# Kernel optimization log

Hardware: AMD Instinct MI355X
Metric: run time of the kernel (lower is better)

Reference implementation:

```python
import jax, jax.numpy as jnp
import numpy as np

B, T, E, D, G = 64, 64, 2048, 4096, 8
H3 = 3 * D  # gru projects deter -> 3*deter (reset, cand, update)
EPS = 1e-4  # Norm default eps


def _rms(x, scale):
    # Norm impl='rms': x * rsqrt(mean(x^2, -1) + eps) * scale
    return x * (jax.lax.rsqrt((x * x).mean(-1, keepdims=True) + EPS) * scale)


def setup_inputs() -> dict:
    key = jax.random.key(0)
    ks = jax.random.split(key, 4)
    x = jax.random.normal(ks[0], (B, T, E), jnp.float32)
    deter0 = jax.random.normal(ks[1], (B, D), jnp.float32)
    # dense in-projection: concat(deter, x) -> D, rms norm + silu
    W_in = jax.random.normal(ks[2], (D + E, D), jnp.float32) * (1.0 / np.sqrt(D + E))
    b_in = jnp.zeros((D,), jnp.float32)
    scale_in = jnp.ones((D,), jnp.float32)
    # BlockLinear D -> 3D with G groups; weight (G, D/G, 3D/G), per-block rms scales
    W_blk = jax.random.normal(ks[3], (G, D // G, H3 // G), jnp.float32) * (1.0 / np.sqrt(D // G))
    b_blk = jnp.zeros((H3,), jnp.float32)
    scale_blk = jnp.ones((G, H3 // G), jnp.float32)
    return dict(x=x, deter0=deter0, W_in=W_in, b_in=b_in, scale_in=scale_in,
                W_blk=W_blk, b_blk=b_blk, scale_blk=scale_blk)


def reference(x, deter0, W_in, b_in, scale_in, W_blk, b_blk, scale_blk):
    def step(deter, x_t):
        h = jnp.concatenate([deter, x_t], -1)                # [B, D+E]
        y = jax.nn.silu(_rms(h @ W_in + b_in, scale_in))     # [B, D]
        # block-diagonal GEMM: '...ki,kio->...ko' as in BlockLinear._layer
        z = jnp.einsum('bgi,gio->bgo', y.reshape(B, G, D // G), W_blk)
        z = z.reshape(B, H3) + b_blk
        # block_norm=True: per-block rms over each of the G contiguous chunks
        z = _rms(z.reshape(B, G, H3 // G), scale_blk).reshape(B, H3)
        reset, cand, update = jnp.split(z, 3, -1)
        reset = jax.nn.sigmoid(reset)
        cand = jnp.tanh(reset * cand)
        update = jax.nn.sigmoid(update - 1.0)
        deter = update * cand + (1.0 - update) * deter
        return deter, deter

    _, deters = jax.lax.scan(step, deter0, jnp.swapaxes(x, 0, 1))  # scan over T
    return jnp.swapaxes(deters, 0, 1)  # [B, T, D]
```

## Files before the change

kernel.cpp:

```cpp
#include <hip/hip_runtime.h>

typedef unsigned short u16;
typedef unsigned int u32;
typedef __bf16 bfx8 __attribute__((ext_vector_type(8)));
typedef float f32x4 __attribute__((ext_vector_type(4)));

constexpr int BB = 64;
constexpr int TT = 64;
constexpr int EE = 2048;
constexpr int DD = 4096;
constexpr int GG = 8;
constexpr int H3 = 3 * DD;
constexpr int CH = H3 / GG;
constexpr float EPSf = 1e-4f;

static __device__ __forceinline__ u16 f2bf(float f) {
  u32 u = __builtin_bit_cast(u32, f);
  u32 r = (u + 0x7fffu + ((u >> 16) & 1u)) >> 16;
  return (u16)r;
}
static __device__ __forceinline__ float bf2f(u16 h) {
  return __builtin_bit_cast(float, (u32)h << 16);
}


__global__ void __launch_bounds__(256) k_f2b(const float* __restrict__ in,
                                             u16* __restrict__ out, int n4) {
  int i = blockIdx.x * 256 + threadIdx.x;
  int stride = gridDim.x * 256;
  for (; i < n4; i += stride) {
    float4 v = ((const float4*)in)[i];
    uint2 o;
    o.x = (u32)f2bf(v.x) | ((u32)f2bf(v.y) << 16);
    o.y = (u32)f2bf(v.z) | ((u32)f2bf(v.w) << 16);
    ((uint2*)out)[i] = o;
  }
}

__global__ void __launch_bounds__(256) k_initdet(const float* __restrict__ d0,
                                                 float* __restrict__ dF,
                                                 u16* __restrict__ dB, int n4) {
  int i = blockIdx.x * 256 + threadIdx.x;
  if (i < n4) {
    float4 v = ((const float4*)d0)[i];
    ((float4*)dF)[i] = v;
    uint2 o;
    o.x = (u32)f2bf(v.x) | ((u32)f2bf(v.y) << 16);
    o.y = (u32)f2bf(v.z) | ((u32)f2bf(v.w) << 16);
    ((uint2*)dB)[i] = o;
  }
}

__global__ void __launch_bounds__(256) k_transpose_f2b(const float* __restrict__ in,
                                                       u16* __restrict__ out,
                                                       int R, int C) {
  __shared__ float tile[32][33];
  size_t base = (size_t)blockIdx.z * R * C;
  in += base; out += base;
  int tx = threadIdx.x & 31, ty = threadIdx.x >> 5;
  int r0 = blockIdx.y * 32, c0 = blockIdx.x * 32;
#pragma unroll
  for (int i = 0; i < 4; i++) {
    int rr = ty * 4 + i;
    tile[rr][tx] = in[(size_t)(r0 + rr) * C + (c0 + tx)];
  }
  __syncthreads();
#pragma unroll
  for (int i = 0; i < 4; i++) {
    int cc = ty * 4 + i;
    out[(size_t)(c0 + cc) * R + (r0 + tx)] = f2bf(tile[tx][cc]);
  }
}

constexpr int P1_LS = 72;
constexpr int P1_BUF = 128 * P1_LS;

__global__ void __launch_bounds__(256) k_p1(const u16* __restrict__ A,
                                            const u16* __restrict__ B,
                                            const float* __restrict__ bias,
                                            u16* __restrict__ C) {
  __shared__ u16 As[2 * P1_BUF];
  __shared__ u16 Bs[2 * P1_BUF];
  const int tid = threadIdx.x;
  const int m0 = blockIdx.y * 128, n0 = blockIdx.x * 128;
  const int w = tid >> 6, lane = tid & 63;
  const int wr = w >> 1, wc = w & 1;
  const int lr = lane & 15, lk = (lane >> 4) * 8, rq = (lane >> 4) * 4;
  const int srow = tid >> 3, scol = (tid & 7) * 8;
  const u16* Ag = A + (size_t)(m0 + srow) * EE + scol;
  const u16* Bg = B + (size_t)(n0 + srow) * (DD + EE) + scol;

  f32x4 acc[4][4] = {};
  uint4 ra[4], rb[4];
#pragma unroll
  for (int i = 0; i < 4; i++) {
    ra[i] = *(const uint4*)(Ag + (size_t)32 * i * EE);
    rb[i] = *(const uint4*)(Bg + (size_t)32 * i * (DD + EE));
  }

  for (int kt = 0; kt < 32; ++kt) {
    const int p = kt & 1;
    u16* ab = As + p * P1_BUF;
    u16* bb = Bs + p * P1_BUF;
#pragma unroll
    for (int i = 0; i < 4; i++) {
      *(uint4*)&ab[(srow + 32 * i) * P1_LS + scol] = ra[i];
      *(uint4*)&bb[(srow + 32 * i) * P1_LS + scol] = rb[i];
    }
    __syncthreads();
    if (kt < 31) {
      const int ko = (kt + 1) * 64;
#pragma unroll
      for (int i = 0; i < 4; i++) {
        ra[i] = *(const uint4*)(Ag + (size_t)32 * i * EE + ko);
        rb[i] = *(const uint4*)(Bg + (size_t)32 * i * (DD + EE) + ko);
      }
    }
#pragma unroll
    for (int kk = 0; kk < 64; kk += 32) {
      bfx8 av[4], bv[4];
#pragma unroll
      for (int mi = 0; mi < 4; mi++)
        av[mi] = *(const bfx8*)&ab[(wr * 64 + mi * 16 + lr) * P1_LS + kk + lk];
#pragma unroll
      for (int ni = 0; ni < 4; ni++)
        bv[ni] = *(const bfx8*)&bb[(wc * 64 + ni * 16 + lr) * P1_LS + kk + lk];
#pragma unroll
      for (int mi = 0; mi < 4; mi++)
#pragma unroll
        for (int ni = 0; ni < 4; ni++)
          acc[mi][ni] = __builtin_amdgcn_mfma_f32_16x16x32_bf16(av[mi], bv[ni], acc[mi][ni], 0, 0, 0);
    }
  }

#pragma unroll
  for (int mi = 0; mi < 4; mi++) {
#pragma unroll
    for (int ni = 0; ni < 4; ni++) {
      const int n = n0 + wc * 64 + ni * 16 + lr;
      const float bias_v = bias[n];
#pragma unroll
      for (int r = 0; r < 4; r++) {
        const int m = m0 + wr * 64 + mi * 16 + rq + r;
        C[(size_t)m * DD + n] = f2bf(acc[mi][ni][r] + bias_v);
      }
    }
  }
}

constexpr int LSA = 136;
constexpr int ABUF = 64 * LSA;

__global__ void __launch_bounds__(512) kA(const u16* __restrict__ dB,
                                          const u16* __restrict__ WT,
                                          float* __restrict__ part) {
  __shared__ u16 As[2 * ABUF];
  __shared__ u16 Bs[2 * ABUF];
  const int tid = threadIdx.x;
  const int n0 = blockIdx.x * 64;
  const int k0 = blockIdx.y * 1024;
  const int w = tid >> 6, lane = tid & 63;
  const int wr = w >> 1, wc = w & 1;
  const int lr = lane & 15, lk = (lane >> 4) * 8, rq = (lane >> 4) * 4;
  const int r0s = tid >> 4, s0 = (tid & 15) * 8;
  const int r1s = r0s + 32;
  const u16* Ag0 = dB + (size_t)r0s * DD + k0 + s0;
  const u16* Ag1 = dB + (size_t)r1s * DD + k0 + s0;
  const u16* Bg0 = WT + (size_t)(n0 + r0s) * (DD + EE) + k0 + s0;
  const u16* Bg1 = WT + (size_t)(n0 + r1s) * (DD + EE) + k0 + s0;
  const int d0 = r0s * LSA + s0, d1 = r1s * LSA + s0;

  f32x4 acc[2] = {};
  uint4 ra0 = *(const uint4*)(Ag0);
  uint4 ra1 = *(const uint4*)(Ag1);
  uint4 rb0 = *(const uint4*)(Bg0);
  uint4 rb1 = *(const uint4*)(Bg1);

  for (int kt = 0; kt < 8; ++kt) {
    const int p = kt & 1;
    u16* ab = As + p * ABUF;
    u16* bb = Bs + p * ABUF;
    *(uint4*)&ab[d0] = ra0;
    *(uint4*)&ab[d1] = ra1;
    *(uint4*)&bb[d0] = rb0;
    *(uint4*)&bb[d1] = rb1;
    __syncthreads();
    if (kt < 7) {
      const int ko = (kt + 1) * 128;
      ra0 = *(const uint4*)(Ag0 + ko);
      ra1 = *(const uint4*)(Ag1 + ko);
      rb0 = *(const uint4*)(Bg0 + ko);
      rb1 = *(const uint4*)(Bg1 + ko);
    }
#pragma unroll
    for (int kk = 0; kk < 128; kk += 32) {
      bfx8 av = *(const bfx8*)&ab[(wr * 16 + lr) * LSA + kk + lk];
#pragma unroll
      for (int ni = 0; ni < 2; ni++) {
        bfx8 bv = *(const bfx8*)&bb[(wc * 32 + ni * 16 + lr) * LSA + kk + lk];
        acc[ni] = __builtin_amdgcn_mfma_f32_16x16x32_bf16(av, bv, acc[ni], 0, 0, 0);
      }
    }
  }

  float* Pp = part + (size_t)blockIdx.y * BB * DD;
#pragma unroll
  for (int ni = 0; ni < 2; ni++)
#pragma unroll
    for (int r = 0; r < 4; r++)
      Pp[(size_t)(wr * 16 + rq + r) * DD + n0 + wc * 32 + ni * 16 + lr] = acc[ni][r];
}

__global__ void __launch_bounds__(256) kB(const float* __restrict__ part,
                                          const u16* __restrict__ Xproj,
                                          const float* __restrict__ scale_in,
                                          u16* __restrict__ ybf, int t) {
  const int b = blockIdx.x, tid = threadIdx.x;
  const int w = tid >> 6, lane = tid & 63;
  __shared__ float sred[4];
  const u16* xp = Xproj + ((size_t)b * TT + t) * DD + tid * 16;
  const float* pb = part + (size_t)b * DD + tid * 16;
  float v[16];
  uint4 x0 = *(const uint4*)(xp);
  uint4 x1 = *(const uint4*)(xp + 8);
#pragma unroll
  for (int j = 0; j < 8; j++) v[j] = bf2f(((const u16*)&x0)[j]);
#pragma unroll
  for (int j = 0; j < 8; j++) v[8 + j] = bf2f(((const u16*)&x1)[j]);
#pragma unroll
  for (int kc = 0; kc < 4; kc++) {
    const float* p = pb + (size_t)kc * BB * DD;
#pragma unroll
    for (int j4 = 0; j4 < 4; j4++) {
      float4 q = *(const float4*)(p + j4 * 4);
      v[j4 * 4 + 0] += q.x; v[j4 * 4 + 1] += q.y;
      v[j4 * 4 + 2] += q.z; v[j4 * 4 + 3] += q.w;
    }
  }
  float ss = 0.f;
#pragma unroll
  for (int j = 0; j < 16; j++) ss += v[j] * v[j];
#pragma unroll
  for (int o = 32; o > 0; o >>= 1) ss += __shfl_down(ss, o);
  if (lane == 0) sred[w] = ss;
  __syncthreads();
  const float r = rsqrtf((sred[0] + sred[1] + sred[2] + sred[3]) / (float)DD + EPSf);
  const float* sc = scale_in + tid * 16;
  uint2 o0, o1;
  u32* po = (u32*)&o0;
#pragma unroll
  for (int j = 0; j < 4; j++) {
    float a = v[2 * j] * r * sc[2 * j];
    float bq = v[2 * j + 1] * r * sc[2 * j + 1];
    a = a / (1.f + __expf(-a)); bq = bq / (1.f + __expf(-bq));
    po[j & 1] = (u32)f2bf(a) | ((u32)f2bf(bq) << 16);
    if (j == 1) *(uint2*)(ybf + (size_t)b * DD + tid * 16) = o0;
  }
  *(uint2*)(ybf + (size_t)b * DD + tid * 16 + 4) = o0;
  u32 pk[8];
#pragma unroll
  for (int j = 0; j < 8; j++) {
    float a = v[2 * j] * r * sc[2 * j];
    float bq = v[2 * j + 1] * r * sc[2 * j + 1];
    a = a / (1.f + __expf(-a)); bq = bq / (1.f + __expf(-bq));
    pk[j] = (u32)f2bf(a) | ((u32)f2bf(bq) << 16);
  }
  uint4 w0 = make_uint4(pk[0], pk[1], pk[2], pk[3]);
  uint4 w1 = make_uint4(pk[4], pk[5], pk[6], pk[7]);
  *(uint4*)(ybf + (size_t)b * DD + tid * 16) = w0;
  *(uint4*)(ybf + (size_t)b * DD + tid * 16 + 8) = w1;
}

constexpr int LSC2 = 72;
constexpr int CBUF = 64 * LSC2;

__global__ void __launch_bounds__(256) kC(const u16* __restrict__ ybf,
                                          const u16* __restrict__ WbT,
                                          const float* __restrict__ b_blk,
                                          float* __restrict__ zbuf,
                                          float* __restrict__ zsq) {
  __shared__ u16 As[2 * CBUF];
  __shared__ u16 Bs[2 * CBUF];
  const int tid = threadIdx.x;
  const int wg = blockIdx.x;
  const int n0g = wg * 64;
  const int g = n0g / CH, nl = n0g % CH;
  const int w = tid >> 6, lane = tid & 63;
  const int lr = lane & 15, lk = (lane >> 4) * 8, rq = (lane >> 4) * 4;
  const int srow = tid >> 2, sc = (tid & 3) * 8;
  const u16* Arow = ybf + (size_t)srow * DD + g * (DD / GG) + sc;
  const u16* Brow = WbT + ((size_t)g * CH + nl + srow) * (DD / GG) + sc;
  const int dA = srow * LSC2 + sc;

  f32x4 acc[4] = {};
  uint4 ra0 = *(const uint4*)(Arow);
  uint4 ra1 = *(const uint4*)(Arow + 32);
  uint4 rb0 = *(const uint4*)(Brow);
  uint4 rb1 = *(const uint4*)(Brow + 32);

  for (int kt = 0; kt < 8; ++kt) {
    const int p = kt & 1;
    u16* ab = As + p * CBUF;
    u16* bb = Bs + p * CBUF;
    *(uint4*)&ab[dA] = ra0;
    *(uint4*)&ab[dA + 32] = ra1;
    *(uint4*)&bb[dA] = rb0;
    *(uint4*)&bb[dA + 32] = rb1;
    __syncthreads();
    if (kt < 7) {
      const int ko = (kt + 1) * 64;
      ra0 = *(const uint4*)(Arow + ko);
      ra1 = *(const uint4*)(Arow + ko + 32);
      rb0 = *(const uint4*)(Brow + ko);
      rb1 = *(const uint4*)(Brow + ko + 32);
    }
#pragma unroll
    for (int kk = 0; kk < 64; kk += 32) {
      bfx8 av = *(const bfx8*)&ab[(w * 16 + lr) * LSC2 + kk + lk];
#pragma unroll
      for (int ni = 0; ni < 4; ni++) {
        bfx8 bv = *(const bfx8*)&bb[(ni * 16 + lr) * LSC2 + kk + lk];
        acc[ni] = __builtin_amdgcn_mfma_f32_16x16x32_bf16(av, bv, acc[ni], 0, 0, 0);
      }
    }
  }

  float sq[4] = {0.f, 0.f, 0.f, 0.f};
#pragma unroll
  for (int ni = 0; ni < 4; ni++) {
    const int n = n0g + ni * 16 + lr;
    const float bias_v = b_blk[n];
#pragma unroll
    for (int r = 0; r < 4; r++) {
      const float zv = acc[ni][r] + bias_v;
      zbuf[(size_t)(w * 16 + rq + r) * H3 + n] = zv;
      sq[r] += zv * zv;
    }
  }
#pragma unroll
  for (int o = 1; o < 16; o <<= 1) {
#pragma unroll
    for (int r = 0; r < 4; r++) sq[r] += __shfl_xor(sq[r], o);
  }
  if (lr == 0) {
#pragma unroll
    for (int r = 0; r < 4; r++) zsq[(size_t)wg * 64 + w * 16 + rq + r] = sq[r];
  }
}

__global__ void __launch_bounds__(256) kD(const float* __restrict__ zbuf,
                                          const float* __restrict__ zsq,
                                          const float* __restrict__ sblk,
                                          float* __restrict__ dF,
                                          u16* __restrict__ dB,
                                          float* __restrict__ out, int t) {
  const int wg = blockIdx.x, tid = threadIdx.x;
  const int b = wg >> 2, s = wg & 3;
  __shared__ float sred[8];
  if (tid < 8) {
    float ssq = 0.f;
    const int j0 = tid * 24;
#pragma unroll
    for (int j = 0; j < 24; j++) ssq += zsq[(size_t)(j0 + j) * 64 + b];
    sred[tid] = rsqrtf(ssq / (float)CH + EPSf);
  }
  __syncthreads();
  const int d0 = s * 1024 + tid * 4;
  const float* zr = zbuf + (size_t)b * H3;
  float4 z0 = *(const float4*)(zr + d0);
  float4 z1 = *(const float4*)(zr + DD + d0);
  float4 z2 = *(const float4*)(zr + 2 * DD + d0);
  float4 dold = *(const float4*)(dF + (size_t)b * DD + d0);
  const float rsA = sred[d0 / CH];
  const float rsB = sred[(DD + d0) / CH];
  const float rsC = sred[(2 * DD + d0) / CH];
  float dn[4];
  const float* z0p = (const float*)&z0;
  const float* z1p = (const float*)&z1;
  const float* z2p = (const float*)&z2;
  const float* dop = (const float*)&dold;
#pragma unroll
  for (int e = 0; e < 4; e++) {
    const int dd = d0 + e;
    const float a0 = z0p[e] * rsA * sblk[dd];
    const float a1 = z1p[e] * rsB * sblk[DD + dd];
    const float a2 = z2p[e] * rsC * sblk[2 * DD + dd];
    const float reset = 1.f / (1.f + __expf(-a0));
    const float cand = tanhf(reset * a1);
    const float upd = 1.f / (1.f + __expf(-(a2 - 1.f)));
    dn[e] = upd * cand + (1.f - upd) * dop[e];
  }
  *(float4*)(dF + (size_t)b * DD + d0) = make_float4(dn[0], dn[1], dn[2], dn[3]);
  uint2 o;
  o.x = (u32)f2bf(dn[0]) | ((u32)f2bf(dn[1]) << 16);
  o.y = (u32)f2bf(dn[2]) | ((u32)f2bf(dn[3]) << 16);
  *(uint2*)(dB + (size_t)b * DD + d0) = o;
  *(float4*)(out + ((size_t)b * TT + t) * DD + d0) = make_float4(dn[0], dn[1], dn[2], dn[3]);
}


extern "C" void kernel_launch(void* const* d_in, const int* in_sizes, int n_in,
                              void* d_out, int out_size, void* d_ws, size_t ws_size,
                              hipStream_t stream) {
  (void)in_sizes; (void)n_in; (void)out_size; (void)ws_size;
  const float* x         = (const float*)d_in[0];
  const float* deter0    = (const float*)d_in[1];
  const float* W_in      = (const float*)d_in[2];
  const float* b_in      = (const float*)d_in[3];
  const float* scale_in  = (const float*)d_in[4];
  const float* W_blk     = (const float*)d_in[5];
  const float* b_blk     = (const float*)d_in[6];
  const float* scale_blk = (const float*)d_in[7];
  float* out = (float*)d_out;

  char* ws = (char*)d_ws;
  size_t off = 0;
  auto alloc = [&](size_t bytes) -> void* {
    void* p = ws + off;
    off += (bytes + 255) & ~(size_t)255;
    return p;
  };
  u16*   WT    = (u16*)alloc((size_t)DD * (DD + EE) * 2);
  u16*   WbT   = (u16*)alloc((size_t)GG * CH * (DD / GG) * 2);
  u16*   Xproj = (u16*)alloc((size_t)BB * TT * DD * 2);
  float* dF    = (float*)alloc((size_t)BB * DD * 4);
  u16*   dB    = (u16*)alloc((size_t)BB * DD * 2);
  char* scratch = (char*)alloc((size_t)BB * TT * EE * 2);
  u16*   xbf  = (u16*)scratch;
  float* part = (float*)scratch;
  size_t o2 = (size_t)4 * BB * DD * 4;
  u16*   ybf  = (u16*)(scratch + o2);
  o2 += (size_t)BB * DD * 2;
  float* zbuf = (float*)(scratch + o2);
  o2 += (size_t)BB * H3 * 4;
  float* zsq  = (float*)(scratch + o2);

  k_f2b<<<dim3(2048), dim3(256), 0, stream>>>(x, xbf, BB * TT * EE / 4);
  k_transpose_f2b<<<dim3(DD / 32, (DD + EE) / 32, 1), dim3(256), 0, stream>>>(W_in, WT, DD + EE, DD);
  k_transpose_f2b<<<dim3(CH / 32, (DD / GG) / 32, GG), dim3(256), 0, stream>>>(W_blk, WbT, DD / GG, CH);
  k_initdet<<<dim3(BB * DD / 4 / 256), dim3(256), 0, stream>>>(deter0, dF, dB, BB * DD / 4);

  k_p1<<<dim3(DD / 128, BB * TT / 128), dim3(256), 0, stream>>>(
      xbf, WT + DD, b_in, Xproj);

  for (int t = 0; t < TT; t++) {
    kA<<<dim3(64, 4), dim3(512), 0, stream>>>(dB, WT, part);
    kB<<<dim3(BB), dim3(256), 0, stream>>>(part, Xproj, scale_in, ybf, t);
    kC<<<dim3(192), dim3(256), 0, stream>>>(ybf, WbT, b_blk, zbuf, zsq);
    kD<<<dim3(256), dim3(256), 0, stream>>>(zbuf, zsq, scale_blk, dF, dB, out, t);
  }
}
```

Baseline: 1.999 ms.

## Fuse per-step recurrent kernels into one persistent kernel with grid barriers

Replaces the 256 per-timestep kernel launches (four kernels times 64 steps) with a single persistent kernel of 256 workgroups. The four phases run in a loop and are separated by atomic-counter grid barriers that are zeroed once up front. Phase A is retiled to 256-thread workgroups covering 64x64 outputs with a 16-step K loop so it matches the common block shape. This removes launch gaps and kernel-boundary drains, but it relies on all 256 workgroups being co-resident and adds spin-wait barrier cost; phase A also loses its 512-thread parallelism.

```diff
diff --git a/kernel.cpp b/kernel.cpp
--- a/kernel.cpp
+++ b/kernel.cpp
@@ -49,6 +49,11 @@
     o.y = (u32)f2bf(v.z) | ((u32)f2bf(v.w) << 16);
     ((uint2*)dB)[i] = o;
   }
+}
+
+__global__ void __launch_bounds__(256) k_zero(int* __restrict__ p, int n) {
+  int i = blockIdx.x * 256 + threadIdx.x;
+  if (i < n) p[i] = 0;
 }
 
 __global__ void __launch_bounds__(256) k_transpose_f2b(const float* __restrict__ in,
@@ -148,149 +153,48 @@
   }
 }
 
-constexpr int LSA = 136;
-constexpr int ABUF = 64 * LSA;
-
-__global__ void __launch_bounds__(512) kA(const u16* __restrict__ dB,
-                                          const u16* __restrict__ WT,
-                                          float* __restrict__ part) {
-  __shared__ u16 As[2 * ABUF];
-  __shared__ u16 Bs[2 * ABUF];
-  const int tid = threadIdx.x;
-  const int n0 = blockIdx.x * 64;
-  const int k0 = blockIdx.y * 1024;
-  const int w = tid >> 6, lane = tid & 63;
-  const int wr = w >> 1, wc = w & 1;
-  const int lr = lane & 15, lk = (lane >> 4) * 8, rq = (lane >> 4) * 4;
-  const int r0s = tid >> 4, s0 = (tid & 15) * 8;
-  const int r1s = r0s + 32;
-  const u16* Ag0 = dB + (size_t)r0s * DD + k0 + s0;
-  const u16* Ag1 = dB + (size_t)r1s * DD + k0 + s0;
-  const u16* Bg0 = WT + (size_t)(n0 + r0s) * (DD + EE) + k0 + s0;
-  const u16* Bg1 = WT + (size_t)(n0 + r1s) * (DD + EE) + k0 + s0;
-  const int d0 = r0s * LSA + s0, d1 = r1s * LSA + s0;
-
-  f32x4 acc[2] = {};
-  uint4 ra0 = *(const uint4*)(Ag0);
-  uint4 ra1 = *(const uint4*)(Ag1);
-  uint4 rb0 = *(const uint4*)(Bg0);
-  uint4 rb1 = *(const uint4*)(Bg1);
-
-  for (int kt = 0; kt < 8; ++kt) {
-    const int p = kt & 1;
-    u16* ab = As + p * ABUF;
-    u16* bb = Bs + p * ABUF;
-    *(uint4*)&ab[d0] = ra0;
-    *(uint4*)&ab[d1] = ra1;
-    *(uint4*)&bb[d0] = rb0;
-    *(uint4*)&bb[d1] = rb1;
-    __syncthreads();
-    if (kt < 7) {
-      const int ko = (kt + 1) * 128;
-      ra0 = *(const uint4*)(Ag0 + ko);
-      ra1 = *(const uint4*)(Ag1 + ko);
-      rb0 = *(const uint4*)(Bg0 + ko);
-      rb1 = *(const uint4*)(Bg1 + ko);
-    }
-#pragma unroll
-    for (int kk = 0; kk < 128; kk += 32) {
-      bfx8 av = *(const bfx8*)&ab[(wr * 16 + lr) * LSA + kk + lk];
-#pragma unroll
-      for (int ni = 0; ni < 2; ni++) {
-        bfx8 bv = *(const bfx8*)&bb[(wc * 32 + ni * 16 + lr) * LSA + kk + lk];
-        acc[ni] = __builtin_amdgcn_mfma_f32_16x16x32_bf16(av, bv, acc[ni], 0, 0, 0);
-      }
-    }
-  }
-
-  float* Pp = part + (size_t)blockIdx.y * BB * DD;
-#pragma unroll
-  for (int ni = 0; ni < 2; ni++)
-#pragma unroll
-    for (int r = 0; r < 4; r++)
-      Pp[(size_t)(wr * 16 + rq + r) * DD + n0 + wc * 32 + ni * 16 + lr] = acc[ni][r];
-}
-
-__global__ void __launch_bounds__(256) kB(const float* __restrict__ part,
-                                          const u16* __restrict__ Xproj,
-                                          const float* __restrict__ scale_in,
-                                          u16* __restrict__ ybf, int t) {
-  const int b = blockIdx.x, tid = threadIdx.x;
-  const int w = tid >> 6, lane = tid & 63;
-  __shared__ float sred[4];
-  const u16* xp = Xproj + ((size_t)b * TT + t) * DD + tid * 16;
-  const float* pb = part + (size_t)b * DD + tid * 16;
-  float v[16];
-  uint4 x0 = *(const uint4*)(xp);
-  uint4 x1 = *(const uint4*)(xp + 8);
-#pragma unroll
-  for (int j = 0; j < 8; j++) v[j] = bf2f(((const u16*)&x0)[j]);
-#pragma unroll
-  for (int j = 0; j < 8; j++) v[8 + j] = bf2f(((const u16*)&x1)[j]);
-#pragma unroll
-  for (int kc = 0; kc < 4; kc++) {
-    const float* p = pb + (size_t)kc * BB * DD;
-#pragma unroll
-    for (int j4 = 0; j4 < 4; j4++) {
-      float4 q = *(const float4*)(p + j4 * 4);
-      v[j4 * 4 + 0] += q.x; v[j4 * 4 + 1] += q.y;
-      v[j4 * 4 + 2] += q.z; v[j4 * 4 + 3] += q.w;
-    }
-  }
-  float ss = 0.f;
-#pragma unroll
-  for (int j = 0; j < 16; j++) ss += v[j] * v[j];
-#pragma unroll
-  for (int o = 32; o > 0; o >>= 1) ss += __shfl_down(ss, o);
-  if (lane == 0) sred[w] = ss;
+
+struct SPc {
+  const u16* WT;
+  const u16* WbT;
+  const u16* Xproj;
+  const float* scale_in;
+  const float* b_blk;
+  const float* sblk;
+  float* part;
+  u16* ybf;
+  float* zbuf;
+  float* zsq;
+  float* dF;
+  u16* dB;
+  float* out;
+  int* bars;
+};
+
+static __device__ __forceinline__ void gbar(int* cnt, int target) {
   __syncthreads();
-  const float r = rsqrtf((sred[0] + sred[1] + sred[2] + sred[3]) / (float)DD + EPSf);
-  const float* sc = scale_in + tid * 16;
-  uint2 o0, o1;
-  u32* po = (u32*)&o0;
-#pragma unroll
-  for (int j = 0; j < 4; j++) {
-    float a = v[2 * j] * r * sc[2 * j];
-    float bq = v[2 * j + 1] * r * sc[2 * j + 1];
-    a = a / (1.f + __expf(-a)); bq = bq / (1.f + __expf(-bq));
-    po[j & 1] = (u32)f2bf(a) | ((u32)f2bf(bq) << 16);
-    if (j == 1) *(uint2*)(ybf + (size_t)b * DD + tid * 16) = o0;
-  }
-  *(uint2*)(ybf + (size_t)b * DD + tid * 16 + 4) = o0;
-  u32 pk[8];
-#pragma unroll
-  for (int j = 0; j < 8; j++) {
-    float a = v[2 * j] * r * sc[2 * j];
-    float bq = v[2 * j + 1] * r * sc[2 * j + 1];
-    a = a / (1.f + __expf(-a)); bq = bq / (1.f + __expf(-bq));
-    pk[j] = (u32)f2bf(a) | ((u32)f2bf(bq) << 16);
-  }
-  uint4 w0 = make_uint4(pk[0], pk[1], pk[2], pk[3]);
-  uint4 w1 = make_uint4(pk[4], pk[5], pk[6], pk[7]);
-  *(uint4*)(ybf + (size_t)b * DD + tid * 16) = w0;
-  *(uint4*)(ybf + (size_t)b * DD + tid * 16 + 8) = w1;
-}
-
-constexpr int LSC2 = 72;
-constexpr int CBUF = 64 * LSC2;
-
-__global__ void __launch_bounds__(256) kC(const u16* __restrict__ ybf,
-                                          const u16* __restrict__ WbT,
-                                          const float* __restrict__ b_blk,
-                                          float* __restrict__ zbuf,
-                                          float* __restrict__ zsq) {
-  __shared__ u16 As[2 * CBUF];
-  __shared__ u16 Bs[2 * CBUF];
-  const int tid = threadIdx.x;
-  const int wg = blockIdx.x;
-  const int n0g = wg * 64;
-  const int g = n0g / CH, nl = n0g % CH;
+  if (threadIdx.x == 0) {
+    __hip_atomic_fetch_add(cnt, 1, __ATOMIC_RELEASE, __HIP_MEMORY_SCOPE_AGENT);
+    while (__hip_atomic_load(cnt, __ATOMIC_RELAXED, __HIP_MEMORY_SCOPE_AGENT) < target)
+      __builtin_amdgcn_s_sleep(4);
+  }
+  __syncthreads();
+  __builtin_amdgcn_fence(__ATOMIC_ACQUIRE, "agent");
+}
+
+constexpr int LSS = 72;
+constexpr int SBUF = 64 * LSS;
+
+static __device__ __forceinline__ void phaseA(const SPc& P, int wg, int tid,
+                                              u16* As, u16* Bs) {
+  const int n0 = (wg & 63) * 64;
+  const int k0 = (wg >> 6) * 1024;
   const int w = tid >> 6, lane = tid & 63;
   const int lr = lane & 15, lk = (lane >> 4) * 8, rq = (lane >> 4) * 4;
   const int srow = tid >> 2, sc = (tid & 3) * 8;
-  const u16* Arow = ybf + (size_t)srow * DD + g * (DD / GG) + sc;
-  const u16* Brow = WbT + ((size_t)g * CH + nl + srow) * (DD / GG) + sc;
-  const int dA = srow * LSC2 + sc;
+  const u16* Arow = P.dB + (size_t)srow * DD + k0 + sc;
+  const u16* Brow = P.WT + (size_t)(n0 + srow) * (DD + EE) + k0 + sc;
+  const int dA = srow * LSS + sc;
 
   f32x4 acc[4] = {};
   uint4 ra0 = *(const uint4*)(Arow);
@@ -298,10 +202,107 @@
   uint4 rb0 = *(const uint4*)(Brow);
   uint4 rb1 = *(const uint4*)(Brow + 32);
 
+  for (int kt = 0; kt < 16; ++kt) {
+    const int p = kt & 1;
+    u16* ab = As + p * SBUF;
+    u16* bb = Bs + p * SBUF;
+    *(uint4*)&ab[dA] = ra0;
+    *(uint4*)&ab[dA + 32] = ra1;
+    *(uint4*)&bb[dA] = rb0;
+    *(uint4*)&bb[dA + 32] = rb1;
+    __syncthreads();
+    if (kt < 15) {
+      const int ko = (kt + 1) * 64;
+      ra0 = *(const uint4*)(Arow + ko);
+      ra1 = *(const uint4*)(Arow + ko + 32);
+      rb0 = *(const uint4*)(Brow + ko);
+      rb1 = *(const uint4*)(Brow + ko + 32);
+    }
+#pragma unroll
+    for (int kk = 0; kk < 64; kk += 32) {
+      bfx8 av = *(const bfx8*)&ab[(w * 16 + lr) * LSS + kk + lk];
+#pragma unroll
+      for (int ni = 0; ni < 4; ni++) {
+        bfx8 bv = *(const bfx8*)&bb[(ni * 16 + lr) * LSS + kk + lk];
+        acc[ni] = __builtin_amdgcn_mfma_f32_16x16x32_bf16(av, bv, acc[ni], 0, 0, 0);
+      }
+    }
+  }
+
+  float* Pp = P.part + (size_t)(wg >> 6) * BB * DD;
+#pragma unroll
+  for (int ni = 0; ni < 4; ni++)
+#pragma unroll
+    for (int r = 0; r < 4; r++)
+      Pp[(size_t)(w * 16 + rq + r) * DD + n0 + ni * 16 + lr] = acc[ni][r];
+}
+
+static __device__ __forceinline__ void phaseB(const SPc& P, int b, int tid, int t,
+                                              float* sred) {
+  const int w = tid >> 6, lane = tid & 63;
+  const u16* xp = P.Xproj + ((size_t)b * TT + t) * DD + tid * 16;
+  const float* pb = P.part + (size_t)b * DD + tid * 16;
+  float v[16];
+  uint4 x0 = *(const uint4*)(xp);
+  uint4 x1 = *(const uint4*)(xp + 8);
+#pragma unroll
+  for (int j = 0; j < 8; j++) {
+    v[j] = bf2f(((const u16*)&x0)[j]);
+    v[8 + j] = bf2f(((const u16*)&x1)[j]);
+  }
+#pragma unroll
+  for (int kc = 0; kc < 4; kc++) {
+    const float* p = pb + (size_t)kc * BB * DD;
+#pragma unroll
+    for (int j4 = 0; j4 < 4; j4++) {
+      float4 q = *(const float4*)(p + j4 * 4);
+      v[j4 * 4 + 0] += q.x; v[j4 * 4 + 1] += q.y;
+      v[j4 * 4 + 2] += q.z; v[j4 * 4 + 3] += q.w;
+    }
+  }
+  float ss = 0.f;
+#pragma unroll
+  for (int j = 0; j < 16; j++) ss += v[j] * v[j];
+#pragma unroll
+  for (int o = 32; o > 0; o >>= 1) ss += __shfl_down(ss, o);
+  if (lane == 0) sred[w] = ss;
+  __syncthreads();
+  const float r = rsqrtf((sred[0] + sred[1] + sred[2] + sred[3]) / (float)DD + EPSf);
+  const float* sc = P.scale_in + tid * 16;
+  u32 pk[8];
+#pragma unroll
+  for (int j = 0; j < 8; j++) {
+    float a = v[2 * j] * r * sc[2 * j];
+    float bq = v[2 * j + 1] * r * sc[2 * j + 1];
+    a = a / (1.f + __expf(-a));
+    bq = bq / (1.f + __expf(-bq));
+    pk[j] = (u32)f2bf(a) | ((u32)f2bf(bq) << 16);
+  }
+  *(uint4*)(P.ybf + (size_t)b * DD + tid * 16) = make_uint4(pk[0], pk[1], pk[2], pk[3]);
+  *(uint4*)(P.ybf + (size_t)b * DD + tid * 16 + 8) = make_uint4(pk[4], pk[5], pk[6], pk[7]);
+}
+
+static __device__ __forceinline__ void phaseC(const SPc& P, int wg, int tid,
+                                              u16* As, u16* Bs) {
+  const int n0g = wg * 64;
+  const int g = wg / 24, nl = n0g - g * CH;
+  const int w = tid >> 6, lane = tid & 63;
+  const int lr = lane & 15, lk = (lane >> 4) * 8, rq = (lane >> 4) * 4;
+  const int srow = tid >> 2, sc = (tid & 3) * 8;
+  const u16* Arow = P.ybf + (size_t)srow * DD + g * (DD / GG) + sc;
+  const u16* Brow = P.WbT + ((size_t)g * CH + nl + srow) * (DD / GG) + sc;
+  const int dA = srow * LSS + sc;
+
+  f32x4 acc[4] = {};
+  uint4 ra0 = *(const uint4*)(Arow);
+  uint4 ra1 = *(const uint4*)(Arow + 32);
+  uint4 rb0 = *(const uint4*)(Brow);
+  uint4 rb1 = *(const uint4*)(Brow + 32);
+
   for (int kt = 0; kt < 8; ++kt) {
     const int p = kt & 1;
-    u16* ab = As + p * CBUF;
-    u16* bb = Bs + p * CBUF;
+    u16* ab = As + p * SBUF;
+    u16* bb = Bs + p * SBUF;
     *(uint4*)&ab[dA] = ra0;
     *(uint4*)&ab[dA + 32] = ra1;
     *(uint4*)&bb[dA] = rb0;
@@ -316,10 +317,10 @@
     }
 #pragma unroll
     for (int kk = 0; kk < 64; kk += 32) {
-      bfx8 av = *(const bfx8*)&ab[(w * 16 + lr) * LSC2 + kk + lk];
+      bfx8 av = *(const bfx8*)&ab[(w * 16 + lr) * LSS + kk + lk];
 #pragma unroll
       for (int ni = 0; ni < 4; ni++) {
-        bfx8 bv = *(const bfx8*)&bb[(ni * 16 + lr) * LSC2 + kk + lk];
+        bfx8 bv = *(const bfx8*)&bb[(ni * 16 + lr) * LSS + kk + lk];
         acc[ni] = __builtin_amdgcn_mfma_f32_16x16x32_bf16(av, bv, acc[ni], 0, 0, 0);
       }
     }
@@ -329,11 +330,11 @@
 #pragma unroll
   for (int ni = 0; ni < 4; ni++) {
     const int n = n0g + ni * 16 + lr;
-    const float bias_v = b_blk[n];
+    const float bias_v = P.b_blk[n];
 #pragma unroll
     for (int r = 0; r < 4; r++) {
       const float zv = acc[ni][r] + bias_v;
-      zbuf[(size_t)(w * 16 + rq + r) * H3 + n] = zv;
+      P.zbuf[(size_t)(w * 16 + rq + r) * H3 + n] = zv;
       sq[r] += zv * zv;
     }
   }
@@ -344,33 +345,27 @@
   }
   if (lr == 0) {
 #pragma unroll
-    for (int r = 0; r < 4; r++) zsq[(size_t)wg * 64 + w * 16 + rq + r] = sq[r];
-  }
-}
-
-__global__ void __launch_bounds__(256) kD(const float* __restrict__ zbuf,
-                                          const float* __restrict__ zsq,
-                                          const float* __restrict__ sblk,
-                                          float* __restrict__ dF,
-                                          u16* __restrict__ dB,
-                                          float* __restrict__ out, int t) {
-  const int wg = blockIdx.x, tid = threadIdx.x;
+    for (int r = 0; r < 4; r++) P.zsq[(size_t)wg * 64 + w * 16 + rq + r] = sq[r];
+  }
+}
+
+static __device__ __forceinline__ void phaseD(const SPc& P, int wg, int tid, int t,
+                                              float* sred) {
   const int b = wg >> 2, s = wg & 3;
-  __shared__ float sred[8];
   if (tid < 8) {
     float ssq = 0.f;
     const int j0 = tid * 24;
 #pragma unroll
-    for (int j = 0; j < 24; j++) ssq += zsq[(size_t)(j0 + j) * 64 + b];
+    for (int j = 0; j < 24; j++) ssq += P.zsq[(size_t)(j0 + j) * 64 + b];
     sred[tid] = rsqrtf(ssq / (float)CH + EPSf);
   }
   __syncthreads();
   const int d0 = s * 1024 + tid * 4;
-  const float* zr = zbuf + (size_t)b * H3;
+  const float* zr = P.zbuf + (size_t)b * H3;
   float4 z0 = *(const float4*)(zr + d0);
   float4 z1 = *(const float4*)(zr + DD + d0);
   float4 z2 = *(const float4*)(zr + 2 * DD + d0);
-  float4 dold = *(const float4*)(dF + (size_t)b * DD + d0);
+  float4 dold = *(const float4*)(P.dF + (size_t)b * DD + d0);
   const float rsA = sred[d0 / CH];
   const float rsB = sred[(DD + d0) / CH];
   const float rsC = sred[(2 * DD + d0) / CH];
@@ -382,20 +377,39 @@
 #pragma unroll
   for (int e = 0; e < 4; e++) {
     const int dd = d0 + e;
-    const float a0 = z0p[e] * rsA * sblk[dd];
-    const float a1 = z1p[e] * rsB * sblk[DD + dd];
-    const float a2 = z2p[e] * rsC * sblk[2 * DD + dd];
+    const float a0 = z0p[e] * rsA * P.sblk[dd];
+    const float a1 = z1p[e] * rsB * P.sblk[DD + dd];
+    const float a2 = z2p[e] * rsC * P.sblk[2 * DD + dd];
     const float reset = 1.f / (1.f + __expf(-a0));
     const float cand = tanhf(reset * a1);
     const float upd = 1.f / (1.f + __expf(-(a2 - 1.f)));
     dn[e] = upd * cand + (1.f - upd) * dop[e];
   }
-  *(float4*)(dF + (size_t)b * DD + d0) = make_float4(dn[0], dn[1], dn[2], dn[3]);
+  *(float4*)(P.dF + (size_t)b * DD + d0) = make_float4(dn[0], dn[1], dn[2], dn[3]);
   uint2 o;
   o.x = (u32)f2bf(dn[0]) | ((u32)f2bf(dn[1]) << 16);
   o.y = (u32)f2bf(dn[2]) | ((u32)f2bf(dn[3]) << 16);
-  *(uint2*)(dB + (size_t)b * DD + d0) = o;
-  *(float4*)(out + ((size_t)b * TT + t) * DD + d0) = make_float4(dn[0], dn[1], dn[2], dn[3]);
+  *(uint2*)(P.dB + (size_t)b * DD + d0) = o;
+  *(float4*)(P.out + ((size_t)b * TT + t) * DD + d0) = make_float4(dn[0], dn[1], dn[2], dn[3]);
+}
+
+__global__ void __launch_bounds__(256) k_scan(SPc P) {
+  __shared__ u16 As[2 * SBUF];
+  __shared__ u16 Bs[2 * SBUF];
+  __shared__ float sred[8];
+  const int wg = blockIdx.x, tid = threadIdx.x;
+
+  for (int t = 0; t < TT; ++t) {
+    int* bt = P.bars + t * 4;
+    phaseA(P, wg, tid, As, Bs);
+    gbar(bt + 0, 256);
+    if (wg < BB) phaseB(P, wg, tid, t, sred);
+    gbar(bt + 1, 256);
+    if (wg < 192) phaseC(P, wg, tid, As, Bs);
+    gbar(bt + 2, 256);
+    phaseD(P, wg, tid, t, sred);
+    gbar(bt + 3, 256);
+  }
 }
 
 
@@ -425,6 +439,7 @@
   u16*   Xproj = (u16*)alloc((size_t)BB * TT * DD * 2);
   float* dF    = (float*)alloc((size_t)BB * DD * 4);
   u16*   dB    = (u16*)alloc((size_t)BB * DD * 2);
+  int*   bars  = (int*)alloc((size_t)TT * 4 * 4);
   char* scratch = (char*)alloc((size_t)BB * TT * EE * 2);
   u16*   xbf  = (u16*)scratch;
   float* part = (float*)scratch;
@@ -439,14 +454,15 @@
   k_transpose_f2b<<<dim3(DD / 32, (DD + EE) / 32, 1), dim3(256), 0, stream>>>(W_in, WT, DD + EE, DD);
   k_transpose_f2b<<<dim3(CH / 32, (DD / GG) / 32, GG), dim3(256), 0, stream>>>(W_blk, WbT, DD / GG, CH);
   k_initdet<<<dim3(BB * DD / 4 / 256), dim3(256), 0, stream>>>(deter0, dF, dB, BB * DD / 4);
+  k_zero<<<dim3(1), dim3(256), 0, stream>>>(bars, TT * 4);
 
   k_p1<<<dim3(DD / 128, BB * TT / 128), dim3(256), 0, stream>>>(
       xbf, WT + DD, b_in, Xproj);
 
-  for (int t = 0; t < TT; t++) {
-    kA<<<dim3(64, 4), dim3(512), 0, stream>>>(dB, WT, part);
-    kB<<<dim3(BB), dim3(256), 0, stream>>>(part, Xproj, scale_in, ybf, t);
-    kC<<<dim3(192), dim3(256), 0, stream>>>(ybf, WbT, b_blk, zbuf, zsq);
-    kD<<<dim3(256), dim3(256), 0, stream>>>(zbuf, zsq, scale_blk, dF, dB, out, t);
-  }
-}
+  SPc SP;
+  SP.WT = WT; SP.WbT = WbT; SP.Xproj = Xproj; SP.scale_in = scale_in;
+  SP.b_blk = b_blk; SP.sblk = scale_blk; SP.part = part; SP.ybf = ybf;
+  SP.zbuf = zbuf; SP.zsq = zsq; SP.dF = dF; SP.dB = dB; SP.out = out;
+  SP.bars = bars;
+  k_scan<<<dim3(256), dim3(256), 0, stream>>>(SP);
+}
```

After: 7.456 ms. 273% more time.
